# Kernel optimization log

Measured on AMD Instinct MI355X. Metric: run time of the kernel, lower is better.

## Reference

```python
import jax, jax.numpy as jnp
import numpy as np

N = 96                      # n_size: neurons per row/column
WAVELENGTH = 1.55e-6        # telecom wavelength (m)
PITCH = 1.55e-6             # neuron spacing = wavelength (m)
Z_SRC = 0.0                 # z of this layer
Z_NEXT = 1e-5               # z of next layer


def setup_inputs() -> dict:
    key = jax.random.key(0)
    k1, k2 = jax.random.split(key)
    x = jax.random.normal(k1, (N, N), dtype=jnp.float32)
    weights = jax.random.normal(k2, (N, N), dtype=jnp.float32)
    coords = (jnp.arange(N, dtype=jnp.float32) - (N - 1) / 2.0) * PITCH
    return {"x": x, "weights": weights, "x_coords": coords, "y_coords": coords}


def reference(x, weights, x_coords, y_coords):
    # Transmission matrix: unit-amplitude, phase = weights  ->  e^{j*w}
    # (weights mod 2*pi gives the same complex value, so exp(1j*w) is exact)
    modes = (jnp.exp(1j * weights) * x).reshape(-1)          # (M,) complex64, M = N*N

    # Neuron grid positions (same x/y grid on both planes, differing only in z)
    xx, yy = jnp.meshgrid(x_coords, y_coords, indexing="ij")
    px = xx.reshape(-1)                                       # (M,)
    py = yy.reshape(-1)                                       # (M,)
    dz = Z_NEXT - Z_SRC

    # Pairwise source->detector distances, (M, M)
    dx = px[:, None] - px[None, :]
    dy = py[:, None] - py[None, :]
    r = jnp.sqrt(dx * dx + dy * dy + dz * dz)

    # First Rayleigh-Sommerfeld diffraction kernel:
    #   w(r) = (dz / r^2) * (1/(2*pi*r) + 1/(j*lambda)) * exp(j*2*pi*r/lambda) * dA
    k = 2.0 * jnp.pi / WAVELENGTH
    g = (dz / (r * r)) * (1.0 / (2.0 * jnp.pi * r) + 1.0 / (1j * WAVELENGTH)) \
        * jnp.exp(1j * k * r)                                 # (M, M) complex64

    dA = PITCH * PITCH
    out = jnp.einsum("i,ij->j", modes, g) * dA                # (M,)
    return out.reshape(N, N)
```

## Files before the change

### kernel.cpp

```cpp
#include <hip/hip_runtime.h>
#include <math.h>


#define NN 96
#define M (NN*NN)
#define GH 191
#define GWG 192
#define GW2 200
#define MW2 104

typedef __attribute__((ext_vector_type(4))) float f32x4;
typedef __attribute__((ext_vector_type(2))) float f32x2;

__device__ float2 g_G[GH * GWG];
__device__ float2 g_modes[M];

__global__ __launch_bounds__(256) void precompute_kernel(
    const float* __restrict__ x, const float* __restrict__ w,
    const float* __restrict__ xc, const float* __restrict__ yc,
    float* __restrict__ out, int out_floats) {
  const double DZ = 1e-5, LAMBDA = 1.55e-6;
  const double TWO_PI     = 6.283185307179586476925;
  const double INV_TWO_PI = 0.15915494309189533577;
  const double K  = TWO_PI / LAMBDA;
  const double DA = LAMBDA * LAMBDA;

  int idx = blockIdx.x * 256 + threadIdx.x;

  if (idx < out_floats) out[idx] = 0.f;

  if (idx < GH * GH) {
    int u = idx / GH - (NN - 1);
    int v = idx % GH - (NN - 1);
    double dx = (double)xc[u < 0 ? -u : u] - (double)xc[0];
    double dy = (double)yc[v < 0 ? -v : v] - (double)yc[0];
    double r2 = dx * dx + dy * dy + DZ * DZ;
    double r  = sqrt(r2);
    double invr2 = 1.0 / r2;
    double amp = DZ * DA * invr2;
    double A = amp * INV_TWO_PI * (r * invr2);
    double B = amp / LAMBDA;
    double ph = K * r;
    double nred = rint(ph * INV_TWO_PI);
    float red = (float)fma(-nred, TWO_PI, ph);
    float s, cs;
    __sincosf(red, &s, &cs);
    g_G[(u + NN - 1) * GWG + (v + NN - 1)] =
        make_float2((float)(A * cs + B * s), (float)(A * s - B * cs));
  } else if (idx < GH * GH + M) {
    int i = idx - GH * GH;
    float s, cs;
    sincosf(w[i], &s, &cs);
    float xv = x[i];
    g_modes[i] = make_float2(cs * xv, s * xv);
  }
}

__global__ __launch_bounds__(192) void conv_kernel(float* __restrict__ out,
                                                   int interleaved) {
  int c  = blockIdx.x;
  int a0 = blockIdx.y * 8;
  int t  = threadIdx.x;

  __shared__ float2 s_modes[8 * MW2];
  __shared__ float2 s_G[8 * GW2 + 8];
  __shared__ float2 s_red[8 * NN];

  #pragma unroll
  for (int k = 0; k < 2; ++k) {
    int idx = k * 192 + t;
    int row = idx / 48, col = idx % 48;
    const float4* src = (const float4*)(g_modes + (a0 + row) * NN);
    ((float4*)(s_modes + row * MW2))[col] = src[col];
  }
  #pragma unroll
  for (int k = 0; k < 4; ++k) {
    int idx = k * 192 + t;
    int row = idx / 96, col = idx % 96;
    const float4* src = (const float4*)(g_G + (a0 + row - c + (NN - 1)) * GWG);
    ((float4*)(s_G + row * GW2))[col] = src[col];
  }
  __syncthreads();

  int q = t % 24;
  int h = t / 24;
  int base = 92 - 4 * q;
  const f32x4* Grow = (const f32x4*)(s_G + h * GW2);
  const f32x4* Mrow = (const f32x4*)(s_modes + h * MW2);
  int gb = base >> 1;

  f32x4 g0 = Grow[gb];
  f32x4 g1 = Grow[gb + 1];
  f32x4 g2 = Grow[gb + 2];
  f32x2 a0c = {0.f, 0.f}, a1c = {0.f, 0.f}, a2c = {0.f, 0.f}, a3c = {0.f, 0.f};

#define LO2(v4) __builtin_shufflevector(v4, v4, 0, 1)
#define HI2(v4) __builtin_shufflevector(v4, v4, 2, 3)

#define CFMA_PK(acc, m2, gg)                                                  \
  asm("v_pk_fma_f32 %0, %1, %2, %0 op_sel:[0,0,0] op_sel_hi:[0,1,1]\n\t"      \
      "v_pk_fma_f32 %0, %1, %2, %0 op_sel:[1,1,0] op_sel_hi:[1,0,1] neg_lo:[0,1,0]" \
      : "+v"(acc) : "v"(m2), "v"(gg))

  #pragma unroll 6
  for (int b = 0; b < NN; b += 2) {
    f32x4 mm = Mrow[b >> 1];
    f32x2 m01 = LO2(mm), m23 = HI2(mm);
    f32x2 g0a = LO2(g0), g0b = HI2(g0);
    f32x2 g1a = LO2(g1), g1b = HI2(g1);
    f32x2 g2a = LO2(g2);
    CFMA_PK(a0c, m01, g1b);
    CFMA_PK(a0c, m23, g2a);
    CFMA_PK(a1c, m01, g1a);
    CFMA_PK(a1c, m23, g1b);
    CFMA_PK(a2c, m01, g0b);
    CFMA_PK(a2c, m23, g1a);
    CFMA_PK(a3c, m01, g0a);
    CFMA_PK(a3c, m23, g0b);
    g0 = g1;
    g1 = g2;
    g2 = Grow[gb + 3 + (b >> 1)];
  }
#undef CFMA_PK
#undef LO2
#undef HI2

  int dbase = 4 * q;
  s_red[h * NN + dbase + 0] = make_float2(a0c.x, a0c.y);
  s_red[h * NN + dbase + 1] = make_float2(a1c.x, a1c.y);
  s_red[h * NN + dbase + 2] = make_float2(a2c.x, a2c.y);
  s_red[h * NN + dbase + 3] = make_float2(a3c.x, a3c.y);
  __syncthreads();

  if (t < NN) {
    float re = 0.f, im = 0.f;
    #pragma unroll
    for (int hh = 0; hh < 8; ++hh) {
      re += s_red[hh * NN + t].x;
      im += s_red[hh * NN + t].y;
    }
    int j = c * NN + t;
    if (interleaved) {
      atomicAdd(out + 2 * j,     re);
      atomicAdd(out + 2 * j + 1, im);
    } else {
      atomicAdd(out + j, re);
    }
  }
}

extern "C" void kernel_launch(void* const* d_in, const int* in_sizes, int n_in,
                              void* d_out, int out_size, void* d_ws, size_t ws_size,
                              hipStream_t stream) {
  const float* x  = (const float*)d_in[0];
  const float* w  = (const float*)d_in[1];
  const float* xc = (const float*)d_in[2];
  const float* yc = (const float*)d_in[3];
  float* out = (float*)d_out;

  int interleaved = (out_size >= 2 * M) ? 1 : 0;
  int out_floats  = interleaved ? 2 * M : M;

  int total = GH * GH + M;
  precompute_kernel<<<(total + 255) / 256, 256, 0, stream>>>(
      x, w, xc, yc, out, out_floats);

  conv_kernel<<<dim3(NN, 12), 192, 0, stream>>>(out, interleaved);
}
```

Baseline: 68.86 us.

## Process 16 source rows per block with 8 outputs per thread

Each block now handles 16 source rows instead of 8, and each thread computes two groups of four output columns that share the same loaded mode values. The grid is halved, so there are half as many atomic adds to global output and half as many redundant G-row loads per output. In exchange, shared memory per block doubles and register pressure rises, and the halved block count (576) may lower occupancy and parallelism on a GPU with many CUs.

```diff
diff --git a/kernel.cpp b/kernel.cpp
--- a/kernel.cpp
+++ b/kernel.cpp
@@ -59,22 +59,22 @@
 __global__ __launch_bounds__(192) void conv_kernel(float* __restrict__ out,
                                                    int interleaved) {
   int c  = blockIdx.x;
-  int a0 = blockIdx.y * 8;
+  int a0 = blockIdx.y * 16;
   int t  = threadIdx.x;
 
-  __shared__ float2 s_modes[8 * MW2];
-  __shared__ float2 s_G[8 * GW2 + 8];
-  __shared__ float2 s_red[8 * NN];
+  __shared__ float2 s_modes[16 * MW2];
+  __shared__ float2 s_G[16 * GW2 + 8];
+  __shared__ float2 s_red[16 * NN];
 
   #pragma unroll
-  for (int k = 0; k < 2; ++k) {
+  for (int k = 0; k < 4; ++k) {
     int idx = k * 192 + t;
     int row = idx / 48, col = idx % 48;
     const float4* src = (const float4*)(g_modes + (a0 + row) * NN);
     ((float4*)(s_modes + row * MW2))[col] = src[col];
   }
   #pragma unroll
-  for (int k = 0; k < 4; ++k) {
+  for (int k = 0; k < 8; ++k) {
     int idx = k * 192 + t;
     int row = idx / 96, col = idx % 96;
     const float4* src = (const float4*)(g_G + (a0 + row - c + (NN - 1)) * GWG);
@@ -82,17 +82,21 @@
   }
   __syncthreads();
 
-  int q = t % 24;
-  int h = t / 24;
-  int base = 92 - 4 * q;
+  int q = t % 12;
+  int h = t / 12;
   const f32x4* Grow = (const f32x4*)(s_G + h * GW2);
   const f32x4* Mrow = (const f32x4*)(s_modes + h * MW2);
-  int gb = base >> 1;
+  int gb1 = 46 - 2 * q;
+  int gb2 = 22 - 2 * q;
 
-  f32x4 g0 = Grow[gb];
-  f32x4 g1 = Grow[gb + 1];
-  f32x4 g2 = Grow[gb + 2];
+  f32x4 p0 = Grow[gb1];
+  f32x4 p1 = Grow[gb1 + 1];
+  f32x4 p2 = Grow[gb1 + 2];
+  f32x4 r0 = Grow[gb2];
+  f32x4 r1 = Grow[gb2 + 1];
+  f32x4 r2 = Grow[gb2 + 2];
   f32x2 a0c = {0.f, 0.f}, a1c = {0.f, 0.f}, a2c = {0.f, 0.f}, a3c = {0.f, 0.f};
+  f32x2 b0c = {0.f, 0.f}, b1c = {0.f, 0.f}, b2c = {0.f, 0.f}, b3c = {0.f, 0.f};
 
 #define LO2(v4) __builtin_shufflevector(v4, v4, 0, 1)
 #define HI2(v4) __builtin_shufflevector(v4, v4, 2, 3)
@@ -106,36 +110,55 @@
   for (int b = 0; b < NN; b += 2) {
     f32x4 mm = Mrow[b >> 1];
     f32x2 m01 = LO2(mm), m23 = HI2(mm);
-    f32x2 g0a = LO2(g0), g0b = HI2(g0);
-    f32x2 g1a = LO2(g1), g1b = HI2(g1);
-    f32x2 g2a = LO2(g2);
-    CFMA_PK(a0c, m01, g1b);
-    CFMA_PK(a0c, m23, g2a);
-    CFMA_PK(a1c, m01, g1a);
-    CFMA_PK(a1c, m23, g1b);
-    CFMA_PK(a2c, m01, g0b);
-    CFMA_PK(a2c, m23, g1a);
-    CFMA_PK(a3c, m01, g0a);
-    CFMA_PK(a3c, m23, g0b);
-    g0 = g1;
-    g1 = g2;
-    g2 = Grow[gb + 3 + (b >> 1)];
+    {
+      f32x2 p0a = LO2(p0), p0b = HI2(p0);
+      f32x2 p1a = LO2(p1), p1b = HI2(p1);
+      f32x2 p2a = LO2(p2);
+      CFMA_PK(a0c, m01, p1b);
+      CFMA_PK(a0c, m23, p2a);
+      CFMA_PK(a1c, m01, p1a);
+      CFMA_PK(a1c, m23, p1b);
+      CFMA_PK(a2c, m01, p0b);
+      CFMA_PK(a2c, m23, p1a);
+      CFMA_PK(a3c, m01, p0a);
+      CFMA_PK(a3c, m23, p0b);
+    }
+    {
+      f32x2 r0a = LO2(r0), r0b = HI2(r0);
+      f32x2 r1a = LO2(r1), r1b = HI2(r1);
+      f32x2 r2a = LO2(r2);
+      CFMA_PK(b0c, m01, r1b);
+      CFMA_PK(b0c, m23, r2a);
+      CFMA_PK(b1c, m01, r1a);
+      CFMA_PK(b1c, m23, r1b);
+      CFMA_PK(b2c, m01, r0b);
+      CFMA_PK(b2c, m23, r1a);
+      CFMA_PK(b3c, m01, r0a);
+      CFMA_PK(b3c, m23, r0b);
+    }
+    p0 = p1; p1 = p2; p2 = Grow[gb1 + 3 + (b >> 1)];
+    r0 = r1; r1 = r2; r2 = Grow[gb2 + 3 + (b >> 1)];
   }
 #undef CFMA_PK
 #undef LO2
 #undef HI2
 
-  int dbase = 4 * q;
-  s_red[h * NN + dbase + 0] = make_float2(a0c.x, a0c.y);
-  s_red[h * NN + dbase + 1] = make_float2(a1c.x, a1c.y);
-  s_red[h * NN + dbase + 2] = make_float2(a2c.x, a2c.y);
-  s_red[h * NN + dbase + 3] = make_float2(a3c.x, a3c.y);
+  int d1 = 4 * q;
+  int d2 = 48 + 4 * q;
+  s_red[h * NN + d1 + 0] = make_float2(a0c.x, a0c.y);
+  s_red[h * NN + d1 + 1] = make_float2(a1c.x, a1c.y);
+  s_red[h * NN + d1 + 2] = make_float2(a2c.x, a2c.y);
+  s_red[h * NN + d1 + 3] = make_float2(a3c.x, a3c.y);
+  s_red[h * NN + d2 + 0] = make_float2(b0c.x, b0c.y);
+  s_red[h * NN + d2 + 1] = make_float2(b1c.x, b1c.y);
+  s_red[h * NN + d2 + 2] = make_float2(b2c.x, b2c.y);
+  s_red[h * NN + d2 + 3] = make_float2(b3c.x, b3c.y);
   __syncthreads();
 
   if (t < NN) {
     float re = 0.f, im = 0.f;
     #pragma unroll
-    for (int hh = 0; hh < 8; ++hh) {
+    for (int hh = 0; hh < 16; ++hh) {
       re += s_red[hh * NN + t].x;
       im += s_red[hh * NN + t].y;
     }
@@ -165,5 +188,5 @@
   precompute_kernel<<<(total + 255) / 256, 256, 0, stream>>>(
       x, w, xc, yc, out, out_floats);
 
-  conv_kernel<<<dim3(NN, 12), 192, 0, stream>>>(out, interleaved);
+  conv_kernel<<<dim3(NN, 6), 192, 0, stream>>>(out, interleaved);
 }
```

New measurement: 72.38 us. 1.05x slower.

## Split conv kernel's source-column loop across a third grid dimension

Applied to the files above, without the earlier changes.

Adds a grid z-dimension of 2 so each block handles half of the 96 source columns (48 instead of 96), which doubles the block count and halves per-block shared loads and loop trip count. The reduction buffer now aliases the G tile in shared memory (with an extra barrier), which lowers LDS use per block and may raise occupancy. The cost is twice as many atomic adds on the output and a clamped G load index at the boundary.

```diff
diff --git a/kernel.cpp b/kernel.cpp
--- a/kernel.cpp
+++ b/kernel.cpp
@@ -6,14 +6,14 @@
 #define M (NN*NN)
 #define GH 191
 #define GWG 192
-#define GW2 200
-#define MW2 104
+#define GW4 76
+#define MW4 26
 
 typedef __attribute__((ext_vector_type(4))) float f32x4;
 typedef __attribute__((ext_vector_type(2))) float f32x2;
 
-__device__ float2 g_G[GH * GWG];
-__device__ float2 g_modes[M];
+__device__ __attribute__((aligned(16))) float2 g_G[GH * GWG];
+__device__ __attribute__((aligned(16))) float2 g_modes[M];
 
 __global__ __launch_bounds__(256) void precompute_kernel(
     const float* __restrict__ x, const float* __restrict__ w,
@@ -60,34 +60,38 @@
                                                    int interleaved) {
   int c  = blockIdx.x;
   int a0 = blockIdx.y * 8;
+  int bh = blockIdx.z;
   int t  = threadIdx.x;
 
-  __shared__ float2 s_modes[8 * MW2];
-  __shared__ float2 s_G[8 * GW2 + 8];
-  __shared__ float2 s_red[8 * NN];
+  __shared__ f32x4 s_G4[8 * GW4];
+  __shared__ f32x4 s_m4[8 * MW4];
+  float2* s_red = (float2*)s_G4;
 
-  #pragma unroll
-  for (int k = 0; k < 2; ++k) {
-    int idx = k * 192 + t;
-    int row = idx / 48, col = idx % 48;
-    const float4* src = (const float4*)(g_modes + (a0 + row) * NN);
-    ((float4*)(s_modes + row * MW2))[col] = src[col];
+  const f32x4* gG4 = (const f32x4*)g_G;
+  const f32x4* gm4 = (const f32x4*)g_modes;
+
+  {
+    int row = t / 24, col = t % 24;
+    s_m4[row * MW4 + col] = gm4[(a0 + row) * 48 + 24 * bh + col];
   }
   #pragma unroll
   for (int k = 0; k < 4; ++k) {
     int idx = k * 192 + t;
-    int row = idx / 96, col = idx % 96;
-    const float4* src = (const float4*)(g_G + (a0 + row - c + (NN - 1)) * GWG);
-    ((float4*)(s_G + row * GW2))[col] = src[col];
+    if (idx < 8 * GW4) {
+      int row = idx / GW4, col = idx % GW4;
+      int grow = a0 + row - c + (NN - 1);
+      int gidx = grow * 96 + 24 * bh + col;
+      if (gidx > GH * 96 - 1) gidx = GH * 96 - 1;
+      s_G4[row * GW4 + col] = gG4[gidx];
+    }
   }
   __syncthreads();
 
   int q = t % 24;
   int h = t / 24;
-  int base = 92 - 4 * q;
-  const f32x4* Grow = (const f32x4*)(s_G + h * GW2);
-  const f32x4* Mrow = (const f32x4*)(s_modes + h * MW2);
-  int gb = base >> 1;
+  const f32x4* Grow = s_G4 + h * GW4;
+  const f32x4* Mrow = s_m4 + h * MW4;
+  int gb = 46 - 2 * q;
 
   f32x4 g0 = Grow[gb];
   f32x4 g1 = Grow[gb + 1];
@@ -103,8 +107,8 @@
       : "+v"(acc) : "v"(m2), "v"(gg))
 
   #pragma unroll 6
-  for (int b = 0; b < NN; b += 2) {
-    f32x4 mm = Mrow[b >> 1];
+  for (int s = 0; s < 24; ++s) {
+    f32x4 mm = Mrow[s];
     f32x2 m01 = LO2(mm), m23 = HI2(mm);
     f32x2 g0a = LO2(g0), g0b = HI2(g0);
     f32x2 g1a = LO2(g1), g1b = HI2(g1);
@@ -119,11 +123,13 @@
     CFMA_PK(a3c, m23, g0b);
     g0 = g1;
     g1 = g2;
-    g2 = Grow[gb + 3 + (b >> 1)];
+    g2 = Grow[gb + 3 + s];
   }
 #undef CFMA_PK
 #undef LO2
 #undef HI2
+
+  __syncthreads();
 
   int dbase = 4 * q;
   s_red[h * NN + dbase + 0] = make_float2(a0c.x, a0c.y);
@@ -165,5 +171,5 @@
   precompute_kernel<<<(total + 255) / 256, 256, 0, stream>>>(
       x, w, xc, yc, out, out_floats);
 
-  conv_kernel<<<dim3(NN, 12), 192, 0, stream>>>(out, interleaved);
+  conv_kernel<<<dim3(NN, 12, 2), 192, 0, stream>>>(out, interleaved);
 }
```

Result: no change. 68.91 us (+0.1%).
